# Optimization experiments

Measured on AMD Instinct MI355X. Metric: run time of the kernel, lower is better.

The kernel has to match this reference:

```python
import jax, jax.numpy as jnp
import numpy as np

D_IN = 256
D_ATTN = 64
STEPS = 2
TOP_P = 0.9
TAU = 1.0
LN_EPS = 1e-5
N_NODES = 8192


def setup_inputs() -> dict:
    key = jax.random.key(0)
    ks = jax.random.split(key, 8)
    N, d, da, steps = N_NODES, D_IN, D_ATTN, STEPS
    X = jax.random.normal(ks[0], (N, d), dtype=jnp.float32)
    S = jax.random.uniform(ks[1], (N, N), dtype=jnp.float32)
    # Linear weights stored torch-style: (out_features, in_features)
    W1 = jax.random.normal(ks[2], (da, d), dtype=jnp.float32) / np.sqrt(d)
    W2 = jax.random.normal(ks[3], (da, da), dtype=jnp.float32) / np.sqrt(da)
    W3 = jax.random.normal(ks[4], (da, d), dtype=jnp.float32) / np.sqrt(d)
    U1 = jax.random.normal(ks[5], (steps, d, d), dtype=jnp.float32) / np.sqrt(d)
    U2 = jax.random.normal(ks[6], (steps, d, d), dtype=jnp.float32) / np.sqrt(d)
    ln_g = jnp.ones((d,), dtype=jnp.float32)
    ln_b = jnp.zeros((d,), dtype=jnp.float32)
    return {"X": X, "S": S, "W1": W1, "W2": W2, "W3": W3,
            "U1": U1, "U2": U2, "ln_g": ln_g, "ln_b": ln_b}


def _top_p_attention(X, W1, W2, W3):
    """Bilinear attention adjacency with nucleus (top-p) sparsification.
    X: (N, d_in) -> A: (N, N) row-stochastic."""
    q = (X @ W1.T) @ W2.T                    # (N, d_attn)
    k = X @ W3.T                             # (N, d_attn)
    logits = (q @ k.T) / TAU                 # (N, N)
    probs = jax.nn.softmax(logits, axis=-1)
    idx = jnp.argsort(-probs, axis=-1)       # descending order indices
    sp = jnp.take_along_axis(probs, idx, axis=-1)
    cs = jnp.cumsum(sp, axis=-1)
    keep_sorted = (cs - sp) < TOP_P          # keep minimal prefix reaching mass p
    rows = jnp.arange(probs.shape[0])[:, None]
    mask = jnp.zeros(probs.shape, dtype=bool).at[rows, idx].set(keep_sorted)
    A = probs * mask
    return A / jnp.maximum(A.sum(-1, keepdims=True), 1e-12)


def reference(X, S, W1, W2, W3, U1, U2, ln_g, ln_b):
    N = X.shape[0]
    # prior: add self-loops, row-normalize
    R = S + jnp.eye(N, dtype=X.dtype)
    R = R / R.sum(-1, keepdims=True)
    Z = jnp.zeros_like(X)
    Xf = X
    Xa = X
    for n in range(STEPS):
        A = _top_p_attention(Xa, W1, W2, W3)
        Xf = R @ Xf                          # prior diffusion
        Xa = A @ Xa                          # adaptive diffusion
        # dropout is eval-mode identity
        Z = Z + Xf @ U1[n].T + Xa @ U2[n].T
    h = X + Z
    mu = h.mean(-1, keepdims=True)
    var = jnp.mean((h - mu) ** 2, axis=-1, keepdims=True)
    return (h - mu) / jnp.sqrt(var + LN_EPS) * ln_g + ln_b
```

## Files before the change

kernel.cpp:

```cpp
#include <hip/hip_runtime.h>
#include <stdint.h>

#define NN 8192
#define D 256
#define DA 64
#define CAND 2048

typedef unsigned short ushort_t;

__device__ float blockSumF(float v, float* scr) {
  __syncthreads();
#pragma unroll
  for (int o = 32; o > 0; o >>= 1) v += __shfl_down(v, o, 64);
  if ((threadIdx.x & 63) == 0) scr[threadIdx.x >> 6] = v;
  __syncthreads();
  return ((scr[0] + scr[1]) + (scr[2] + scr[3]));
}
__device__ float blockMaxF(float v, float* scr) {
  __syncthreads();
#pragma unroll
  for (int o = 32; o > 0; o >>= 1) v = fmaxf(v, __shfl_down(v, o, 64));
  if ((threadIdx.x & 63) == 0) scr[threadIdx.x >> 6] = v;
  __syncthreads();
  return fmaxf(fmaxf(scr[0], scr[1]), fmaxf(scr[2], scr[3]));
}
__device__ float blockScanIncl(float v, float* wscr) {
#pragma unroll
  for (int off = 1; off < 64; off <<= 1) {
    float u = __shfl_up(v, off, 64);
    if ((threadIdx.x & 63) >= off) v += u;
  }
  __syncthreads();
  if ((threadIdx.x & 63) == 63) wscr[threadIdx.x >> 6] = v;
  __syncthreads();
  float add = 0.0f;
  int wid = threadIdx.x >> 6;
  for (int w = 0; w < wid; w++) add += wscr[w];
  return v + add;
}

__global__ void zero_kernel(float* __restrict__ p, size_t n) {
  for (size_t i = (size_t)blockIdx.x * blockDim.x + threadIdx.x; i < n;
       i += (size_t)gridDim.x * blockDim.x)
    p[i] = 0.0f;
}

__global__ __launch_bounds__(256) void rowsum_kernel(const float* __restrict__ S, float* __restrict__ den) {
  __shared__ float scr[4];
  int row = blockIdx.x, tid = threadIdx.x;
  const float* sr = S + (size_t)row * NN;
  float s = 0;
  for (int c = tid * 4; c < NN; c += 1024) {
    float4 u = *(const float4*)(sr + c);
    s += (u.x + u.y) + (u.z + u.w);
  }
  float tot = blockSumF(s, scr);
  if (tid == 0) den[row] = tot + 1.0f;
}

__global__ __launch_bounds__(256) void xf_gemm(const float* __restrict__ S,
                                               const float* __restrict__ XfC,
                                               const float* __restrict__ den,
                                               float* __restrict__ XfN) {
  __shared__ float Ast[64][68];
  __shared__ float Bs[64][68];
  int tid = threadIdx.x;
  int tx = tid & 15, ty = tid >> 4;
  int rb = blockIdx.x * 64;
  int cb = blockIdx.y * 64;
  float acc[4][4] = {};
  for (int kt = 0; kt < NN; kt += 64) {
    for (int i = tid; i < 4096; i += 256) {
      int r = i >> 6, c = i & 63;
      Ast[c][r] = S[(size_t)(rb + r) * NN + kt + c];
      Bs[r][c] = XfC[(size_t)(kt + r) * D + cb + c];
    }
    __syncthreads();
#pragma unroll 8
    for (int k = 0; k < 64; k++) {
      float4 av = *(const float4*)&Ast[k][ty * 4];
      float4 bv = *(const float4*)&Bs[k][tx * 4];
      acc[0][0] = fmaf(av.x, bv.x, acc[0][0]); acc[0][1] = fmaf(av.x, bv.y, acc[0][1]);
      acc[0][2] = fmaf(av.x, bv.z, acc[0][2]); acc[0][3] = fmaf(av.x, bv.w, acc[0][3]);
      acc[1][0] = fmaf(av.y, bv.x, acc[1][0]); acc[1][1] = fmaf(av.y, bv.y, acc[1][1]);
      acc[1][2] = fmaf(av.y, bv.z, acc[1][2]); acc[1][3] = fmaf(av.y, bv.w, acc[1][3]);
      acc[2][0] = fmaf(av.z, bv.x, acc[2][0]); acc[2][1] = fmaf(av.z, bv.y, acc[2][1]);
      acc[2][2] = fmaf(av.z, bv.z, acc[2][2]); acc[2][3] = fmaf(av.z, bv.w, acc[2][3]);
      acc[3][0] = fmaf(av.w, bv.x, acc[3][0]); acc[3][1] = fmaf(av.w, bv.y, acc[3][1]);
      acc[3][2] = fmaf(av.w, bv.z, acc[3][2]); acc[3][3] = fmaf(av.w, bv.w, acc[3][3]);
    }
    __syncthreads();
  }
#pragma unroll
  for (int i = 0; i < 4; i++) {
    int r = rb + ty * 4 + i;
    float dinv = 1.0f / den[r];
#pragma unroll
    for (int j = 0; j < 4; j++) {
      int c = cb + tx * 4 + j;
      XfN[(size_t)r * D + c] = (acc[i][j] + XfC[(size_t)r * D + c]) * dinv;
    }
  }
}

__global__ __launch_bounds__(64) void qk32_kernel(const float* __restrict__ Xa,
    const float* __restrict__ W1, const float* __restrict__ W2, const float* __restrict__ W3,
    float* __restrict__ qf, float* __restrict__ kf) {
  __shared__ float x[D];
  __shared__ float ts[DA];
  int row = blockIdx.x, tid = threadIdx.x;
  for (int i = tid; i < D; i += 64) x[i] = Xa[(size_t)row * D + i];
  __syncthreads();
  const float* w1r = W1 + (size_t)tid * D;
  const float* w3r = W3 + (size_t)tid * D;
  float t = 0.0f, kv = 0.0f;
  for (int d = 0; d < D; d++) {
    float xv = x[d];
    t  = fmaf(xv, w1r[d], t);
    kv = fmaf(xv, w3r[d], kv);
  }
  kf[(size_t)row * DA + tid] = kv;
  ts[tid] = t;
  __syncthreads();
  const float* w2r = W2 + (size_t)tid * DA;
  float qv = 0.0f;
  for (int a = 0; a < DA; a++) qv = fmaf(ts[a], w2r[a], qv);
  qf[(size_t)row * DA + tid] = qv;
}

__global__ __launch_bounds__(256) void logits32(const float* __restrict__ qf,
    const float* __restrict__ kf, float* __restrict__ L, int rowBase) {
  __shared__ float qs[64][65];
  __shared__ float ks[64][65];
  int tid = threadIdx.x;
  int tx = tid & 15, ty = tid >> 4;
  int colTile = blockIdx.x * 64;
  int rowTile = blockIdx.y * 64;
  for (int i = tid; i < 4096; i += 256) {
    int r = i >> 6, c = i & 63;
    qs[c][r] = qf[(size_t)(rowBase + rowTile + r) * DA + c];
    ks[c][r] = kf[(size_t)(colTile + r) * DA + c];
  }
  __syncthreads();
  float acc[4][4] = {};
  for (int c = 0; c < 64; c++) {
    float a0 = qs[c][ty * 4], a1 = qs[c][ty * 4 + 1];
    float a2 = qs[c][ty * 4 + 2], a3 = qs[c][ty * 4 + 3];
    float b0 = ks[c][tx * 4], b1 = ks[c][tx * 4 + 1];
    float b2 = ks[c][tx * 4 + 2], b3 = ks[c][tx * 4 + 3];
    acc[0][0] = fmaf(a0, b0, acc[0][0]); acc[0][1] = fmaf(a0, b1, acc[0][1]);
    acc[0][2] = fmaf(a0, b2, acc[0][2]); acc[0][3] = fmaf(a0, b3, acc[0][3]);
    acc[1][0] = fmaf(a1, b0, acc[1][0]); acc[1][1] = fmaf(a1, b1, acc[1][1]);
    acc[1][2] = fmaf(a1, b2, acc[1][2]); acc[1][3] = fmaf(a1, b3, acc[1][3]);
    acc[2][0] = fmaf(a2, b0, acc[2][0]); acc[2][1] = fmaf(a2, b1, acc[2][1]);
    acc[2][2] = fmaf(a2, b2, acc[2][2]); acc[2][3] = fmaf(a2, b3, acc[2][3]);
    acc[3][0] = fmaf(a3, b0, acc[3][0]); acc[3][1] = fmaf(a3, b1, acc[3][1]);
    acc[3][2] = fmaf(a3, b2, acc[3][2]); acc[3][3] = fmaf(a3, b3, acc[3][3]);
  }
#pragma unroll
  for (int i = 0; i < 4; i++)
#pragma unroll
    for (int j = 0; j < 4; j++)
      L[(size_t)(rowTile + ty * 4 + i) * NN + colTile + tx * 4 + j] = acc[i][j];
}

__global__ __launch_bounds__(256) void topp_histsel(const float* __restrict__ L,
    const float* __restrict__ XaOld, float* __restrict__ XaNew, int rowBase) {
  __shared__ float ps[NN];
  __shared__ float hsum[256];
  __shared__ float hcntf[256];
  __shared__ float cv[CAND];
  __shared__ ushort_t ci[CAND];
  __shared__ float wsum[4][256];
  __shared__ float wscr[4];
  __shared__ float scr[4];
  __shared__ float zsh;
  __shared__ unsigned sh_lo, sh_hi, sh_tie;
  __shared__ float sh_M, sh_asum, sh_hs;
  __shared__ int sh_C, sh_cross, sh_hc, sh_icut, sh_nkt, sh_ntot, sh_cnt;

  int tid = threadIdx.x;
  const float* Lr = L + (size_t)blockIdx.x * NN;
  float lm = -INFINITY;
  for (int c = tid * 4; c < NN; c += 1024) {
    float4 u = *(const float4*)(Lr + c);
    ps[c] = u.x; ps[c + 1] = u.y; ps[c + 2] = u.z; ps[c + 3] = u.w;
    lm = fmaxf(fmaxf(lm, fmaxf(u.x, u.y)), fmaxf(u.z, u.w));
  }
  float m = blockMaxF(lm, scr);
  if (tid < 64) {
    int base = tid * 128;
    float r[8];
#pragma unroll
    for (int j = 0; j < 8; j++) r[j] = expf(ps[base + j] - m);
    for (int i = 8; i < 128; i += 8)
#pragma unroll
      for (int j = 0; j < 8; j++) r[j] += expf(ps[base + i + j] - m);
    float leaf = ((r[0] + r[1]) + (r[2] + r[3])) + ((r[4] + r[5]) + (r[6] + r[7]));
#pragma unroll
    for (int off = 1; off < 64; off <<= 1) leaf += __shfl_down(leaf, off, 64);
    if (tid == 0) zsh = leaf;
  }
  hsum[tid] = 0.0f; hcntf[tid] = 0.0f;
  if (tid == 0) { sh_M = 0.0f; sh_C = 0; sh_cross = 256; }
  __syncthreads();
  float z = zsh;
  for (int j = tid; j < NN; j += 256) {
    float p = expf(ps[j] - m) / z;
    ps[j] = p;
    int b = (int)(__float_as_uint(p) >> 20) - 768;
    if (b >= 0) { atomicAdd(&hsum[b], p); atomicAdd(&hcntf[b], 1.0f); }
  }
  __syncthreads();
  for (int lev = 0; lev < 4; lev++) {
    float x  = hsum[255 - tid];
    float xc = hcntf[255 - tid];
    float inclm = blockScanIncl(x, wscr);
    float inclc = blockScanIncl(xc, wscr);
    if (sh_M + inclm >= 0.9f) atomicMin(&sh_cross, tid);
    __syncthreads();
    int ct = sh_cross; if (ct == 256) ct = 255;
    if (tid == ct) {
      int key = 255 - tid;
      sh_M = sh_M + (inclm - x);
      sh_C = sh_C + (int)(inclc - xc + 0.5f);
      sh_hs = x; sh_hc = (int)(xc + 0.5f);
      unsigned nlo, nhi;
      if (lev == 0) { nlo = (unsigned)(768 + key) << 20; nhi = nlo + (1u << 20); }
      else {
        int s = (lev == 1) ? 12 : (lev == 2) ? 4 : 0;
        nlo = sh_lo + ((unsigned)key << s); nhi = nlo + (1u << s);
      }
      sh_lo = nlo; sh_hi = nhi;
    }
    __syncthreads();
    if (sh_hc == 1 || lev == 3) break;
    hsum[tid] = 0.0f; hcntf[tid] = 0.0f;
    if (tid == 0) sh_cross = 256;
    __syncthreads();
    unsigned rlo = sh_lo, rhi = sh_hi;
    int s2 = (lev == 0) ? 12 : (lev == 1) ? 4 : 0;
    unsigned msk = (lev == 2) ? 15u : 255u;
    for (int j = tid; j < NN; j += 256) {
      unsigned u = __float_as_uint(ps[j]);
      if (u >= rlo && u < rhi) {
        unsigned key = (u >> s2) & msk;
        atomicAdd(&hsum[key], ps[j]); atomicAdd(&hcntf[key], 1.0f);
      }
    }
    __syncthreads();
  }
  if (tid == 0) {
    if (sh_hc == 1) {
      sh_tie = sh_lo; sh_nkt = 1; sh_asum = sh_M + sh_hs; sh_icut = NN;
    } else {
      float tiev = __uint_as_float(sh_lo);
      float cs = sh_M; int n = 0; int nt = sh_hc;
      while (n < nt && cs < 0.9f) { cs += tiev; n++; }
      sh_tie = sh_lo; sh_nkt = n; sh_asum = cs;
      sh_icut = (n == nt) ? NN : ((n == 0) ? -1 : -2);
    }
    sh_ntot = sh_C + sh_nkt;
    sh_cnt = 0;
  }
  __syncthreads();
  if (sh_icut == -2) {
    int need = sh_nkt; unsigned tb = sh_tie;
    int lo_ = 0, hi_ = NN - 1;
    for (int it = 0; it < 13; it++) {
      int mid = (lo_ + hi_) >> 1;
      float c = 0.0f;
      for (int j = tid; j < NN; j += 256)
        if (__float_as_uint(ps[j]) == tb && j <= mid) c += 1.0f;
      c = blockSumF(c, scr);
      if (c >= (float)need) hi_ = mid; else lo_ = mid + 1;
    }
    if (tid == 0) sh_icut = hi_;
    __syncthreads();
  }
  unsigned tie = sh_tie; int icut = sh_icut;
  float asum = fmaxf(sh_asum, 1e-12f);
  int ntot = sh_ntot;
  int wid = tid >> 6, lane = tid & 63;
  float4 acc; acc.x = acc.y = acc.z = acc.w = 0.0f;
  if (ntot <= CAND) {
    for (int j = tid; j < NN; j += 256) {
      float p = ps[j]; unsigned u = __float_as_uint(p);
      if (u > tie || (u == tie && j <= icut)) {
        int s = atomicAdd(&sh_cnt, 1);
        cv[s] = p; ci[s] = (ushort_t)j;
      }
    }
    __syncthreads();
    int nc = sh_cnt;
    for (int i = wid; i < nc; i += 4) {
      float pw = cv[i] / asum;
      const float4 xv = *(const float4*)(XaOld + (size_t)ci[i] * D + lane * 4);
      acc.x = fmaf(pw, xv.x, acc.x); acc.y = fmaf(pw, xv.y, acc.y);
      acc.z = fmaf(pw, xv.z, acc.z); acc.w = fmaf(pw, xv.w, acc.w);
    }
  } else {
    for (int j = wid; j < NN; j += 4) {
      float p = ps[j]; unsigned u = __float_as_uint(p);
      if (u > tie || (u == tie && j <= icut)) {
        float pw = p / asum;
        const float4 xv = *(const float4*)(XaOld + (size_t)j * D + lane * 4);
        acc.x = fmaf(pw, xv.x, acc.x); acc.y = fmaf(pw, xv.y, acc.y);
        acc.z = fmaf(pw, xv.z, acc.z); acc.w = fmaf(pw, xv.w, acc.w);
      }
    }
    __syncthreads();
  }
  *(float4*)&wsum[wid][lane * 4] = acc;
  __syncthreads();
  int col = tid;
  float o = (wsum[0][col] + wsum[1][col]) + (wsum[2][col] + wsum[3][col]);
  XaNew[(size_t)(rowBase + blockIdx.x) * D + col] = o;
}

__global__ __launch_bounds__(256) void z_accum(const float* __restrict__ Xf, const float* __restrict__ Xa,
    const float* __restrict__ U1n, const float* __restrict__ U2n, float* __restrict__ Z) {
  __shared__ float xf[4][D];
  __shared__ float xa[4][D];
  int r0 = blockIdx.x * 4, tid = threadIdx.x;
  for (int i = tid; i < 4 * D; i += 256) {
    xf[i >> 8][i & 255] = Xf[(size_t)r0 * D + i];
    xa[i >> 8][i & 255] = Xa[(size_t)r0 * D + i];
  }
  __syncthreads();
  const float* u1r = U1n + (size_t)tid * D;
  const float* u2r = U2n + (size_t)tid * D;
  float a0 = 0, a1 = 0, a2 = 0, a3 = 0, b0 = 0, b1 = 0, b2 = 0, b3 = 0;
  for (int d = 0; d < D; d += 4) {
    float4 u1 = *(const float4*)(u1r + d);
    float4 u2 = *(const float4*)(u2r + d);
    float f1[4] = {u1.x, u1.y, u1.z, u1.w};
    float f2[4] = {u2.x, u2.y, u2.z, u2.w};
#pragma unroll
    for (int j = 0; j < 4; j++) {
      int dd = d + j;
      a0 += xf[0][dd] * f1[j]; a1 += xf[1][dd] * f1[j];
      a2 += xf[2][dd] * f1[j]; a3 += xf[3][dd] * f1[j];
      b0 += xa[0][dd] * f2[j]; b1 += xa[1][dd] * f2[j];
      b2 += xa[2][dd] * f2[j]; b3 += xa[3][dd] * f2[j];
    }
  }
  Z[(size_t)(r0 + 0) * D + tid] += a0 + b0;
  Z[(size_t)(r0 + 1) * D + tid] += a1 + b1;
  Z[(size_t)(r0 + 2) * D + tid] += a2 + b2;
  Z[(size_t)(r0 + 3) * D + tid] += a3 + b3;
}

__global__ __launch_bounds__(256) void ln_kernel(const float* __restrict__ X, const float* __restrict__ Z,
    const float* __restrict__ g, const float* __restrict__ bb, float* __restrict__ out) {
  __shared__ float scr[4];
  int row = blockIdx.x, tid = threadIdx.x;
  float h = X[(size_t)row * D + tid] + Z[(size_t)row * D + tid];
  float mu = blockSumF(h, scr) * (1.0f / 256.0f);
  float dv = h - mu;
  float var = blockSumF(dv * dv, scr) * (1.0f / 256.0f);
  float o = dv / sqrtf(var + 1e-5f) * g[tid] + bb[tid];
  out[(size_t)row * D + tid] = o;
}

extern "C" void kernel_launch(void* const* d_in, const int* in_sizes, int n_in,
                              void* d_out, int out_size, void* d_ws, size_t ws_size,
                              hipStream_t stream) {
  const float* X  = (const float*)d_in[0];
  const float* S  = (const float*)d_in[1];
  const float* W1 = (const float*)d_in[2];
  const float* W2 = (const float*)d_in[3];
  const float* W3 = (const float*)d_in[4];
  const float* U1 = (const float*)d_in[5];
  const float* U2 = (const float*)d_in[6];
  const float* g  = (const float*)d_in[7];
  const float* b  = (const float*)d_in[8];

  char* w = (char*)d_ws;
  size_t off = 0;
  auto alloc = [&](size_t bytes) {
    void* p = w + off; off += (bytes + 255) & ~(size_t)255; return p;
  };
  float* A1  = (float*)alloc((size_t)NN * D * 4);
  float* A2  = (float*)alloc((size_t)NN * D * 4);
  float* F1  = (float*)alloc((size_t)NN * D * 4);
  float* F2  = (float*)alloc((size_t)NN * D * 4);
  float* Z   = (float*)alloc((size_t)NN * D * 4);
  float* den = (float*)alloc((size_t)NN * 4);
  float* qf  = (float*)alloc((size_t)NN * DA * 4);
  float* kf  = (float*)alloc((size_t)NN * DA * 4);
  int chunk = 512;
  while (chunk > 64 && off + (size_t)chunk * NN * 4 + 4096 > ws_size) chunk >>= 1;
  float* L32 = (float*)alloc((size_t)chunk * NN * 4);
  (void)in_sizes; (void)n_in; (void)out_size;

  zero_kernel<<<1024, 256, 0, stream>>>(Z, (size_t)NN * D);
  rowsum_kernel<<<NN, 256, 0, stream>>>(S, den);

  const float* XaC = X;  float* XaN = A1;
  const float* XfC = X;  float* XfN = F1;
  for (int n = 0; n < 2; n++) {
    xf_gemm<<<dim3(128, 4), 256, 0, stream>>>(S, XfC, den, XfN);
    qk32_kernel<<<NN, 64, 0, stream>>>(XaC, W1, W2, W3, qf, kf);
    for (int c = 0; c < NN / chunk; c++) {
      logits32<<<dim3(NN / 64, chunk / 64), 256, 0, stream>>>(qf, kf, L32, c * chunk);
      topp_histsel<<<chunk, 256, 0, stream>>>(L32, XaC, XaN, c * chunk);
    }
    z_accum<<<2048, 256, 0, stream>>>(XfN, XaN, U1 + (size_t)n * D * D, U2 + (size_t)n * D * D, Z);
    XaC = XaN; XaN = A2;
    XfC = XfN; XfN = F2;
  }
  ln_kernel<<<NN, 256, 0, stream>>>(X, Z, g, b, (float*)d_out);
}
```

Before: 6.081 ms.

## Enlarge xf_gemm tile with register prefetch and swizzled LDS; fuse softmax exp pass

The S·Xf GEMM now uses 128-row tiles with 8x4 accumulators per thread, loads S and Xf as float4 into registers one k-tile ahead, and writes them to an XOR-swizzled transposed LDS layout to avoid bank conflicts. This is meant to cut global-load latency stalls and raise arithmetic intensity, at the cost of more registers and half the blocks (256). In top-p selection, the separate single-wavefront exp-sum pass is removed: unnormalized exponentials are computed once, histogrammed, and summed together, with the 0.9 threshold scaled by Z. This changes the histogram bucketing from normalized to unnormalized probabilities, which may shift which values fall into the tracked bins.

New measurement: 6.415 ms. +5.5%, slower.

```diff
diff --git a/kernel.cpp b/kernel.cpp
--- a/kernel.cpp
+++ b/kernel.cpp
@@ -5,6 +5,8 @@
 #define D 256
 #define DA 64
 #define CAND 2048
+#define BMX 128
+#define BKX 64
 
 typedef unsigned short ushort_t;
 
@@ -62,38 +64,85 @@
                                                const float* __restrict__ XfC,
                                                const float* __restrict__ den,
                                                float* __restrict__ XfN) {
-  __shared__ float Ast[64][68];
-  __shared__ float Bs[64][68];
+  __shared__ float Ast[BKX][BMX];
+  __shared__ float Bs[BKX][68];
   int tid = threadIdx.x;
   int tx = tid & 15, ty = tid >> 4;
-  int rb = blockIdx.x * 64;
+  int rb = blockIdx.x * BMX;
   int cb = blockIdx.y * 64;
-  float acc[4][4] = {};
-  for (int kt = 0; kt < NN; kt += 64) {
-    for (int i = tid; i < 4096; i += 256) {
-      int r = i >> 6, c = i & 63;
-      Ast[c][r] = S[(size_t)(rb + r) * NN + kt + c];
-      Bs[r][c] = XfC[(size_t)(kt + r) * D + cb + c];
-    }
-    __syncthreads();
+  float acc[8][4] = {};
+  float4 aR[8], bR[4];
+  int c4 = tid & 15;
+
+#define STAGE_ISSUE(kt)                                                        \
+  {                                                                            \
+    _Pragma("unroll")                                                          \
+    for (int t = 0; t < 8; t++) {                                              \
+      int i4 = tid + 256 * t; int r = i4 >> 4;                                 \
+      aR[t] = *(const float4*)(S + (size_t)(rb + r) * NN + (kt) + c4 * 4);     \
+    }                                                                          \
+    _Pragma("unroll")                                                          \
+    for (int t = 0; t < 4; t++) {                                              \
+      int i4 = tid + 256 * t; int r = i4 >> 4;                                 \
+      bR[t] = *(const float4*)(XfC + (size_t)((kt) + r) * D + cb + c4 * 4);    \
+    }                                                                          \
+  }
+#define STAGE_WRITE()                                                          \
+  {                                                                            \
+    int sw = c4 << 3;                                                          \
+    _Pragma("unroll")                                                          \
+    for (int t = 0; t < 8; t++) {                                              \
+      int i4 = tid + 256 * t; int rp = (i4 >> 4) ^ sw;                         \
+      Ast[4 * c4 + 0][rp] = aR[t].x;                                           \
+      Ast[4 * c4 + 1][rp] = aR[t].y;                                           \
+      Ast[4 * c4 + 2][rp] = aR[t].z;                                           \
+      Ast[4 * c4 + 3][rp] = aR[t].w;                                           \
+    }                                                                          \
+    _Pragma("unroll")                                                          \
+    for (int t = 0; t < 4; t++) {                                              \
+      int i4 = tid + 256 * t; int r = i4 >> 4;                                 \
+      *(float4*)(&Bs[r][c4 * 4]) = bR[t];                                      \
+    }                                                                          \
+  }
+
+  STAGE_ISSUE(0);
+  STAGE_WRITE();
+  __syncthreads();
+  for (int kt = 0; kt < NN; kt += BKX) {
+    if (kt + BKX < NN) STAGE_ISSUE(kt + BKX);
 #pragma unroll 8
-    for (int k = 0; k < 64; k++) {
-      float4 av = *(const float4*)&Ast[k][ty * 4];
+    for (int k = 0; k < BKX; k++) {
+      int sw = ((k >> 2) & 15) << 3;
+      int ra = (ty * 8) ^ sw;
+      float4 a0 = *(const float4*)&Ast[k][ra];
+      float4 a1 = *(const float4*)&Ast[k][ra + 4];
       float4 bv = *(const float4*)&Bs[k][tx * 4];
-      acc[0][0] = fmaf(av.x, bv.x, acc[0][0]); acc[0][1] = fmaf(av.x, bv.y, acc[0][1]);
-      acc[0][2] = fmaf(av.x, bv.z, acc[0][2]); acc[0][3] = fmaf(av.x, bv.w, acc[0][3]);
-      acc[1][0] = fmaf(av.y, bv.x, acc[1][0]); acc[1][1] = fmaf(av.y, bv.y, acc[1][1]);
-      acc[1][2] = fmaf(av.y, bv.z, acc[1][2]); acc[1][3] = fmaf(av.y, bv.w, acc[1][3]);
-      acc[2][0] = fmaf(av.z, bv.x, acc[2][0]); acc[2][1] = fmaf(av.z, bv.y, acc[2][1]);
-      acc[2][2] = fmaf(av.z, bv.z, acc[2][2]); acc[2][3] = fmaf(av.z, bv.w, acc[2][3]);
-      acc[3][0] = fmaf(av.w, bv.x, acc[3][0]); acc[3][1] = fmaf(av.w, bv.y, acc[3][1]);
-      acc[3][2] = fmaf(av.w, bv.z, acc[3][2]); acc[3][3] = fmaf(av.w, bv.w, acc[3][3]);
-    }
-    __syncthreads();
-  }
-#pragma unroll
-  for (int i = 0; i < 4; i++) {
-    int r = rb + ty * 4 + i;
+      acc[0][0] = fmaf(a0.x, bv.x, acc[0][0]); acc[0][1] = fmaf(a0.x, bv.y, acc[0][1]);
+      acc[0][2] = fmaf(a0.x, bv.z, acc[0][2]); acc[0][3] = fmaf(a0.x, bv.w, acc[0][3]);
+      acc[1][0] = fmaf(a0.y, bv.x, acc[1][0]); acc[1][1] = fmaf(a0.y, bv.y, acc[1][1]);
+      acc[1][2] = fmaf(a0.y, bv.z, acc[1][2]); acc[1][3] = fmaf(a0.y, bv.w, acc[1][3]);
+      acc[2][0] = fmaf(a0.z, bv.x, acc[2][0]); acc[2][1] = fmaf(a0.z, bv.y, acc[2][1]);
+      acc[2][2] = fmaf(a0.z, bv.z, acc[2][2]); acc[2][3] = fmaf(a0.z, bv.w, acc[2][3]);
+      acc[3][0] = fmaf(a0.w, bv.x, acc[3][0]); acc[3][1] = fmaf(a0.w, bv.y, acc[3][1]);
+      acc[3][2] = fmaf(a0.w, bv.z, acc[3][2]); acc[3][3] = fmaf(a0.w, bv.w, acc[3][3]);
+      acc[4][0] = fmaf(a1.x, bv.x, acc[4][0]); acc[4][1] = fmaf(a1.x, bv.y, acc[4][1]);
+      acc[4][2] = fmaf(a1.x, bv.z, acc[4][2]); acc[4][3] = fmaf(a1.x, bv.w, acc[4][3]);
+      acc[5][0] = fmaf(a1.y, bv.x, acc[5][0]); acc[5][1] = fmaf(a1.y, bv.y, acc[5][1]);
+      acc[5][2] = fmaf(a1.y, bv.z, acc[5][2]); acc[5][3] = fmaf(a1.y, bv.w, acc[5][3]);
+      acc[6][0] = fmaf(a1.z, bv.x, acc[6][0]); acc[6][1] = fmaf(a1.z, bv.y, acc[6][1]);
+      acc[6][2] = fmaf(a1.z, bv.z, acc[6][2]); acc[6][3] = fmaf(a1.z, bv.w, acc[6][3]);
+      acc[7][0] = fmaf(a1.w, bv.x, acc[7][0]); acc[7][1] = fmaf(a1.w, bv.y, acc[7][1]);
+      acc[7][2] = fmaf(a1.w, bv.z, acc[7][2]); acc[7][3] = fmaf(a1.w, bv.w, acc[7][3]);
+    }
+    __syncthreads();
+    if (kt + BKX < NN) {
+      STAGE_WRITE();
+    }
+    __syncthreads();
+  }
+#pragma unroll
+  for (int i = 0; i < 8; i++) {
+    int r = rb + ty * 8 + i;
     float dinv = 1.0f / den[r];
 #pragma unroll
     for (int j = 0; j < 4; j++) {
@@ -101,6 +150,8 @@
       XfN[(size_t)r * D + c] = (acc[i][j] + XfC[(size_t)r * D + c]) * dinv;
     }
   }
+#undef STAGE_ISSUE
+#undef STAGE_WRITE
 }
 
 __global__ __launch_bounds__(64) void qk32_kernel(const float* __restrict__ Xa,
@@ -174,7 +225,6 @@
   __shared__ float wsum[4][256];
   __shared__ float wscr[4];
   __shared__ float scr[4];
-  __shared__ float zsh;
   __shared__ unsigned sh_lo, sh_hi, sh_tie;
   __shared__ float sh_M, sh_asum, sh_hs;
   __shared__ int sh_C, sh_cross, sh_hc, sh_icut, sh_nkt, sh_ntot, sh_cnt;
@@ -184,40 +234,38 @@
   float lm = -INFINITY;
   for (int c = tid * 4; c < NN; c += 1024) {
     float4 u = *(const float4*)(Lr + c);
-    ps[c] = u.x; ps[c + 1] = u.y; ps[c + 2] = u.z; ps[c + 3] = u.w;
+    *(float4*)(ps + c) = u;
     lm = fmaxf(fmaxf(lm, fmaxf(u.x, u.y)), fmaxf(u.z, u.w));
   }
   float m = blockMaxF(lm, scr);
-  if (tid < 64) {
-    int base = tid * 128;
-    float r[8];
-#pragma unroll
-    for (int j = 0; j < 8; j++) r[j] = expf(ps[base + j] - m);
-    for (int i = 8; i < 128; i += 8)
-#pragma unroll
-      for (int j = 0; j < 8; j++) r[j] += expf(ps[base + i + j] - m);
-    float leaf = ((r[0] + r[1]) + (r[2] + r[3])) + ((r[4] + r[5]) + (r[6] + r[7]));
-#pragma unroll
-    for (int off = 1; off < 64; off <<= 1) leaf += __shfl_down(leaf, off, 64);
-    if (tid == 0) zsh = leaf;
-  }
   hsum[tid] = 0.0f; hcntf[tid] = 0.0f;
   if (tid == 0) { sh_M = 0.0f; sh_C = 0; sh_cross = 256; }
   __syncthreads();
-  float z = zsh;
-  for (int j = tid; j < NN; j += 256) {
-    float p = expf(ps[j] - m) / z;
-    ps[j] = p;
-    int b = (int)(__float_as_uint(p) >> 20) - 768;
-    if (b >= 0) { atomicAdd(&hsum[b], p); atomicAdd(&hcntf[b], 1.0f); }
-  }
-  __syncthreads();
+  float zp = 0.0f;
+  for (int c = tid * 4; c < NN; c += 1024) {
+    float4 u = *(const float4*)(ps + c);
+    float4 ev;
+    ev.x = expf(u.x - m); ev.y = expf(u.y - m);
+    ev.z = expf(u.z - m); ev.w = expf(u.w - m);
+    *(float4*)(ps + c) = ev;
+    zp += (ev.x + ev.y) + (ev.z + ev.w);
+    int b0 = (int)(__float_as_uint(ev.x) >> 20) - 768;
+    if (b0 >= 0) { atomicAdd(&hsum[b0], ev.x); atomicAdd(&hcntf[b0], 1.0f); }
+    int b1 = (int)(__float_as_uint(ev.y) >> 20) - 768;
+    if (b1 >= 0) { atomicAdd(&hsum[b1], ev.y); atomicAdd(&hcntf[b1], 1.0f); }
+    int b2 = (int)(__float_as_uint(ev.z) >> 20) - 768;
+    if (b2 >= 0) { atomicAdd(&hsum[b2], ev.z); atomicAdd(&hcntf[b2], 1.0f); }
+    int b3 = (int)(__float_as_uint(ev.w) >> 20) - 768;
+    if (b3 >= 0) { atomicAdd(&hsum[b3], ev.w); atomicAdd(&hcntf[b3], 1.0f); }
+  }
+  float Z = blockSumF(zp, scr);
+  float thr = 0.9f * Z;
   for (int lev = 0; lev < 4; lev++) {
     float x  = hsum[255 - tid];
     float xc = hcntf[255 - tid];
     float inclm = blockScanIncl(x, wscr);
     float inclc = blockScanIncl(xc, wscr);
-    if (sh_M + inclm >= 0.9f) atomicMin(&sh_cross, tid);
+    if (sh_M + inclm >= thr) atomicMin(&sh_cross, tid);
     __syncthreads();
     int ct = sh_cross; if (ct == 256) ct = 255;
     if (tid == ct) {
@@ -256,7 +304,7 @@
     } else {
       float tiev = __uint_as_float(sh_lo);
       float cs = sh_M; int n = 0; int nt = sh_hc;
-      while (n < nt && cs < 0.9f) { cs += tiev; n++; }
+      while (n < nt && cs < thr) { cs += tiev; n++; }
       sh_tie = sh_lo; sh_nkt = n; sh_asum = cs;
       sh_icut = (n == nt) ? NN : ((n == 0) ? -1 : -2);
     }
@@ -400,7 +448,7 @@
   const float* XaC = X;  float* XaN = A1;
   const float* XfC = X;  float* XfN = F1;
   for (int n = 0; n < 2; n++) {
-    xf_gemm<<<dim3(128, 4), 256, 0, stream>>>(S, XfC, den, XfN);
+    xf_gemm<<<dim3(NN / BMX, 4), 256, 0, stream>>>(S, XfC, den, XfN);
     qk32_kernel<<<NN, 64, 0, stream>>>(XaC, W1, W2, W3, qf, kf);
     for (int c = 0; c < NN / chunk; c++) {
       logits32<<<dim3(NN / 64, chunk / 64), 256, 0, stream>>>(qf, kf, L32, c * chunk);
```
